# Optimization experiments

Hardware: AMD Instinct MI355X
Metric: run time of the kernel (lower is better)

The kernel has to match this reference:

```python
import jax, jax.numpy as jnp
import numpy as np

K_ORDER = 3
GRID_N = 10
GRID_LO, GRID_HI = -2.0, 2.0
LAYERS = [(49, 256), (256, 256), (256, 10)]
NCOEF = GRID_N + K_ORDER  # 13


def mish(x):
    return x * jnp.tanh(jax.nn.softplus(x))


def bspline_basis(x):
    # x: (B, in) -> basis (B, in, GRID_N + K_ORDER)
    h = (GRID_HI - GRID_LO) / GRID_N
    knots = GRID_LO + h * jnp.arange(-K_ORDER, GRID_N + K_ORDER + 1, dtype=x.dtype)  # (G+2k+1,)
    xx = x[..., None]
    B = ((xx >= knots[:-1]) & (xx < knots[1:])).astype(x.dtype)  # degree-0, (B,in,G+2k)
    for d in range(1, K_ORDER + 1):
        left = (xx - knots[: -(d + 1)]) / (knots[d:-1] - knots[: -(d + 1)]) * B[..., :-1]
        right = (knots[d + 1:] - xx) / (knots[d + 1:] - knots[1:-d]) * B[..., 1:]
        B = left + right
    return B  # (B, in, G+k)


def kan_layer(x, coef, scale_base, scale_sp, bias):
    # x: (B,in); coef: (in,out,G+k); scales: (in,out); bias: (out,)
    basis = bspline_basis(x)                                   # (B,in,G+k)
    spline = jnp.einsum('big,iog->bo', basis, coef * scale_sp[..., None])
    base = jnp.einsum('bi,io->bo', mish(x), scale_base)
    return base + spline + bias


def setup_inputs() -> dict:
    key = jax.random.key(0)
    ks = jax.random.split(key, 1 + 4 * len(LAYERS))
    inp = {'x': jax.random.normal(ks[0], (8192, 1, 28, 28), dtype=jnp.float32)}
    i = 1
    for li, (fin, fout) in enumerate(LAYERS, start=1):
        inp[f'coef{li}'] = 0.1 * jax.random.normal(ks[i], (fin, fout, NCOEF), dtype=jnp.float32); i += 1
        inp[f'sb{li}'] = 1.0 + 0.1 * jax.random.normal(ks[i], (fin, fout), dtype=jnp.float32); i += 1
        inp[f'sp{li}'] = 1.0 + 0.1 * jax.random.normal(ks[i], (fin, fout), dtype=jnp.float32); i += 1
        inp[f'b{li}'] = jnp.zeros((fout,), dtype=jnp.float32); i += 1
    return inp


def reference(x, coef1, sb1, sp1, b1, coef2, sb2, sp2, b2, coef3, sb3, sp3, b3):
    B = x.shape[0]
    # avg_pool2d(x, 4): 28x28 -> 7x7
    h = x.reshape(B, 1, 7, 4, 7, 4).mean(axis=(3, 5))
    h = h.reshape(B, 49)
    h = kan_layer(h, coef1, sb1, sp1, b1)
    h = kan_layer(h, coef2, sb2, sp2, b2)
    h = kan_layer(h, coef3, sb3, sp3, b3)
    return jax.nn.log_softmax(h, axis=1)
```

## Files before the change

kernel.cpp:

```cpp
#include <hip/hip_runtime.h>
#include <hip/hip_bf16.h>

typedef __bf16 bf16x8_t __attribute__((ext_vector_type(8)));
typedef float f32x4_t __attribute__((ext_vector_type(4)));
using bf16 = __hip_bfloat16;

__device__ __forceinline__ unsigned short f2bf_bits(float v) {
  __hip_bfloat16 h = __float2bfloat16(v);
  return *reinterpret_cast<unsigned short*>(&h);
}

__device__ __forceinline__ float mish_f(float x) {
  float z = __expf(x);
  float n = z * (z + 2.0f);
  float m = x * n / (n + 2.0f);
  return (x > 10.0f) ? x : m;
}

__device__ __forceinline__ void kan_feats28(bf16* dst, float x) {
  unsigned int* d32 = (unsigned int*)dst;
#pragma unroll
  for (int d = 0; d < 7; ++d) d32[d] = 0u;
  float t = (x + 3.2f) * 2.5f;
  if (t >= 0.0f && t < 16.0f) {
    float tf = floorf(t);
    int c = (int)tf;
    float u = t - tf;
    float um = 1.0f - u;
    float u2 = u * u, u3 = u2 * u;
    const float s6 = 1.0f / 6.0f;
    float w0 = um * um * um * s6;
    float w1 = (3.0f * u3 - 6.0f * u2 + 4.0f) * s6;
    float w2 = (-3.0f * u3 + 3.0f * u2 + 3.0f * u + 1.0f) * s6;
    float w3 = u3 * s6;
    int j0 = c - 3;
    if (j0 >= 0)               dst[j0]     = __float2bfloat16(w0);
    if (j0 >= -1 && j0 <= 11)  dst[j0 + 1] = __float2bfloat16(w1);
    if (j0 >= -2 && j0 <= 10)  dst[j0 + 2] = __float2bfloat16(w2);
    if (j0 <= 9)               dst[j0 + 3] = __float2bfloat16(w3);
  }
  dst[13] = __float2bfloat16(mish_f(x));
}

__global__ __launch_bounds__(256) void prep_all(
    const float* __restrict__ c1, const float* __restrict__ sb1, const float* __restrict__ sp1,
    const float* __restrict__ c2, const float* __restrict__ sb2, const float* __restrict__ sp2,
    const float* __restrict__ c3, const float* __restrict__ sb3, const float* __restrict__ sp3,
    bf16* __restrict__ W1f, bf16* __restrict__ W2f, bf16* __restrict__ W3f) {
  const int b = blockIdx.x, o = threadIdx.x;
  float vals[14];
  const int ntg = o >> 4, lrr = o & 15;
  if (b < 49) {
    const int i = b;
    const size_t io = (size_t)i * 256 + o;
    const float spv = sp1[io];
#pragma unroll
    for (int r = 0; r < 13; ++r) vals[r] = c1[io * 13 + r] * spv;
    vals[13] = sb1[io];
#pragma unroll
    for (int d = 0; d < 7; ++d) {
      const int k2 = i * 14 + 2 * d;
      const int s = k2 >> 5, r2 = k2 & 31;
      const size_t off = ((size_t)(s * 16 + ntg)) * 512 + lrr * 32 + (r2 >> 3) * 8 + (r2 & 7);
      *(unsigned int*)(W1f + off) = (unsigned int)f2bf_bits(vals[2 * d]) |
                                    ((unsigned int)f2bf_bits(vals[2 * d + 1]) << 16);
    }
  } else if (b == 49) {
#pragma unroll
    for (int d = 0; d < 9; ++d) {
      const int k2 = 686 + 2 * d;
      const int r2 = k2 & 31;
      *(unsigned int*)(W1f + ((size_t)(21 * 16 + ntg)) * 512 + lrr * 32 + (r2 >> 3) * 8 + (r2 & 7)) = 0u;
    }
  } else if (b < 306) {
    const int i = b - 50;
    const size_t io = (size_t)i * 256 + o;
    const float spv = sp2[io];
#pragma unroll
    for (int r = 0; r < 13; ++r) vals[r] = c2[io * 13 + r] * spv;
    vals[13] = sb2[io];
#pragma unroll
    for (int d = 0; d < 7; ++d) {
      const int k2 = i * 14 + 2 * d;
      const int s = k2 >> 5, r2 = k2 & 31;
      const size_t off = ((size_t)(s * 16 + ntg)) * 512 + lrr * 32 + (r2 >> 3) * 8 + (r2 & 7);
      *(unsigned int*)(W2f + off) = (unsigned int)f2bf_bits(vals[2 * d]) |
                                    ((unsigned int)f2bf_bits(vals[2 * d + 1]) << 16);
    }
  } else {
    const int i = b - 306;
    if (o < 10) {
      const size_t io = (size_t)i * 10 + o;
      const float spv = sp3[io];
#pragma unroll
      for (int r = 0; r < 13; ++r) vals[r] = c3[io * 13 + r] * spv;
      vals[13] = sb3[io];
#pragma unroll
      for (int d = 0; d < 7; ++d) {
        const int k2 = i * 14 + 2 * d;
        const int s = k2 >> 5, r2 = k2 & 31;
        const size_t off = (size_t)s * 512 + o * 32 + (r2 >> 3) * 8 + (r2 & 7);
        *(unsigned int*)(W3f + off) = (unsigned int)f2bf_bits(vals[2 * d]) |
                                      ((unsigned int)f2bf_bits(vals[2 * d + 1]) << 16);
      }
    } else if (o < 16) {
#pragma unroll
      for (int d = 0; d < 7; ++d) {
        const int k2 = i * 14 + 2 * d;
        const int s = k2 >> 5, r2 = k2 & 31;
        *(unsigned int*)(W3f + (size_t)s * 512 + o * 32 + (r2 >> 3) * 8 + (r2 & 7)) = 0u;
      }
    }
  }
}

__global__ __launch_bounds__(1024, 4) void meganet(
    const float* __restrict__ x, const bf16* __restrict__ W1f,
    const bf16* __restrict__ W2f, const bf16* __restrict__ W3f,
    const float* __restrict__ b1, const float* __restrict__ b2,
    const float* __restrict__ b3, float* __restrict__ out) {
  __shared__ __align__(16) char lds[126976];
  float* const Hs0 = (float*)lds;
  float* const Hs1 = (float*)(lds + 36864);
  bf16* const Ach0 = (bf16*)(lds + 73728);
  bf16* const Ach1 = (bf16*)(lds + 88576);
  float* const P = (float*)(lds + 103424);
  float* const xs = (float*)lds;
  float* const Red = (float*)(lds + 110592);
  float* const V = (float*)(lds + 124928);

  const int t = threadIdx.x;
  const int w = t >> 6, lane = t & 63, quad = lane >> 4, lr = lane & 15;
  const int tr = (t >> 4) & 31, ej = t & 15;
  const int r0 = blockIdx.x * 32;
  const int foff = lr * 32 + quad * 8;
  const int kg = w >> 3, ng = w & 7;
  const int ntg0 = 2 * ng;
  const int nks = kg ? 3 : 4, ks0 = kg ? 4 : 0;

  for (int h = 0; h < 2; ++h) {
    const float4* src = (const float4*)x + (size_t)(r0 + h * 16) * 196;
    float4* xd = (float4*)xs;
#pragma unroll
    for (int l = 0; l < 4; ++l) {
      const int idx = t + l * 1024;
      if (idx < 3136) xd[idx] = src[idx];
    }
    __syncthreads();
    if (t < 784) {
      const int img = t / 49, p = t - img * 49;
      const int oh = p / 7, ow = p - oh * 7;
      const float* xi = xs + img * 784 + oh * 112 + ow * 4;
      float s = 0.f;
#pragma unroll
      for (int rr = 0; rr < 4; ++rr)
#pragma unroll
        for (int cc = 0; cc < 4; ++cc) s += xi[rr * 28 + cc];
      P[(h * 16 + img) * 56 + p] = s * (1.0f / 16.0f);
    }
    __syncthreads();
  }

  f32x4_t acc[2][2];
#pragma unroll
  for (int m = 0; m < 2; ++m)
#pragma unroll
    for (int n = 0; n < 2; ++n) acc[m][n] = (f32x4_t){0.f, 0.f, 0.f, 0.f};

  bf16x8_t q0[4], q1[4];
  if (kg == 0) {
#pragma unroll
    for (int s = 0; s < 4; ++s) {
      q0[s] = *(const bf16x8_t*)(W1f + (size_t)(s * 16 + ntg0) * 512 + foff);
      q1[s] = *(const bf16x8_t*)(W1f + (size_t)(s * 16 + ntg0 + 1) * 512 + foff);
    }
  }
  if (t >= 512) kan_feats28(Ach0 + tr * 232 + ej * 14, P[tr * 56 + ej]);
  __syncthreads();
#pragma unroll
  for (int c = 0; c < 4; ++c) {
    const bf16* const Ac = (c & 1) ? Ach1 : Ach0;
    bf16* const An = (c & 1) ? Ach0 : Ach1;
    const int nksc = (c < 3) ? 7 : 1;
    if (kg == 0) {
#pragma unroll
      for (int ks = 0; ks < 7; ++ks) {
        if (ks >= nksc) continue;
        const int kk = c * 7 + ks;
        const int sl = kk & 3;
        bf16x8_t bb0 = q0[sl], bb1 = q1[sl];
        if (kk + 4 < 22) {
          q0[sl] = *(const bf16x8_t*)(W1f + (size_t)((kk + 4) * 16 + ntg0) * 512 + foff);
          q1[sl] = *(const bf16x8_t*)(W1f + (size_t)((kk + 4) * 16 + ntg0 + 1) * 512 + foff);
        }
#pragma unroll
        for (int m = 0; m < 2; ++m) {
          bf16x8_t a = *(const bf16x8_t*)(Ac + (m * 16 + lr) * 232 + ks * 32 + quad * 8);
          acc[m][0] = __builtin_amdgcn_mfma_f32_16x16x32_bf16(a, bb0, acc[m][0], 0, 0, 0);
          acc[m][1] = __builtin_amdgcn_mfma_f32_16x16x32_bf16(a, bb1, acc[m][1], 0, 0, 0);
        }
      }
    }
    if (t >= 512) {
      if (c < 2) {
        kan_feats28(An + tr * 232 + ej * 14, P[tr * 56 + (c + 1) * 16 + ej]);
      } else if (c == 2) {
        if (ej == 0) kan_feats28(An + tr * 232, P[tr * 56 + 48]);
        else if (ej == 1) {
          unsigned int* z = (unsigned int*)(An + tr * 232 + 14);
#pragma unroll
          for (int d = 0; d < 9; ++d) z[d] = 0u;
        }
      }
    }
    __syncthreads();
  }
  if (kg == 0) {
#pragma unroll
    for (int m = 0; m < 2; ++m)
#pragma unroll
      for (int n = 0; n < 2; ++n) {
        const int col = ng * 32 + n * 16 + lr;
        const float bn = b1[col];
        f32x4_t v;
#pragma unroll
        for (int r = 0; r < 4; ++r) v[r] = acc[m][n][r] + bn;
        *(f32x4_t*)(Hs0 + col * 36 + m * 16 + quad * 4) = v;
      }
  }
  __syncthreads();

#pragma unroll
  for (int m = 0; m < 2; ++m)
#pragma unroll
    for (int n = 0; n < 2; ++n) acc[m][n] = (f32x4_t){0.f, 0.f, 0.f, 0.f};
  bf16x8_t c0[4], c1[4];
#pragma unroll
  for (int j = 0; j < 4; ++j) {
    if (j < nks) {
      const int kk = ks0 + j;
      c0[j] = *(const bf16x8_t*)(W2f + (size_t)(kk * 16 + ntg0) * 512 + foff);
      c1[j] = *(const bf16x8_t*)(W2f + (size_t)(kk * 16 + ntg0 + 1) * 512 + foff);
    }
  }
  if (t >= 512) kan_feats28(Ach0 + tr * 232 + ej * 14, Hs0[ej * 36 + tr]);
  __syncthreads();
#pragma unroll
  for (int c = 0; c < 16; ++c) {
    const bf16* const Ac = (c & 1) ? Ach1 : Ach0;
    bf16* const An = (c & 1) ? Ach0 : Ach1;
#pragma unroll
    for (int j = 0; j < 4; ++j) {
      if (j >= nks) continue;
      const int kk = c * 7 + ks0 + j;
      bf16x8_t bb0 = c0[j], bb1 = c1[j];
      if (c < 15) {
        c0[j] = *(const bf16x8_t*)(W2f + (size_t)((kk + 7) * 16 + ntg0) * 512 + foff);
        c1[j] = *(const bf16x8_t*)(W2f + (size_t)((kk + 7) * 16 + ntg0 + 1) * 512 + foff);
      }
#pragma unroll
      for (int m = 0; m < 2; ++m) {
        bf16x8_t a = *(const bf16x8_t*)(Ac + (m * 16 + lr) * 232 + (ks0 + j) * 32 + quad * 8);
        acc[m][0] = __builtin_amdgcn_mfma_f32_16x16x32_bf16(a, bb0, acc[m][0], 0, 0, 0);
        acc[m][1] = __builtin_amdgcn_mfma_f32_16x16x32_bf16(a, bb1, acc[m][1], 0, 0, 0);
      }
    }
    if (t >= 512 && c < 15)
      kan_feats28(An + tr * 232 + ej * 14, Hs0[((c + 1) * 16 + ej) * 36 + tr]);
    __syncthreads();
  }
  {
    float* const Hd = kg ? Hs1 : Hs0;
#pragma unroll
    for (int m = 0; m < 2; ++m)
#pragma unroll
      for (int n = 0; n < 2; ++n) {
        const int col = ng * 32 + n * 16 + lr;
        const float bn = kg ? 0.f : b2[col];
        f32x4_t v;
#pragma unroll
        for (int r = 0; r < 4; ++r) v[r] = acc[m][n][r] + bn;
        *(f32x4_t*)(Hd + col * 36 + m * 16 + quad * 4) = v;
      }
  }
  __syncthreads();

  f32x4_t acc3 = {0.f, 0.f, 0.f, 0.f};
  const int mh = w / 7, ks3 = w % 7;
  bf16x8_t q3[2];
  if (w < 14) {
    q3[0] = *(const bf16x8_t*)(W3f + (size_t)ks3 * 512 + foff);
    q3[1] = *(const bf16x8_t*)(W3f + (size_t)(7 + ks3) * 512 + foff);
  }
  if (t < 512) kan_feats28(Ach0 + tr * 232 + ej * 14, Hs0[ej * 36 + tr] + Hs1[ej * 36 + tr]);
  __syncthreads();
#pragma unroll
  for (int c = 0; c < 16; ++c) {
    const bf16* const Ac = (c & 1) ? Ach1 : Ach0;
    bf16* const An = (c & 1) ? Ach0 : Ach1;
    if (w < 14) {
      bf16x8_t bb = q3[c & 1];
      if (c + 2 < 16)
        q3[c & 1] = *(const bf16x8_t*)(W3f + (size_t)((c + 2) * 7 + ks3) * 512 + foff);
      bf16x8_t a = *(const bf16x8_t*)(Ac + (mh * 16 + lr) * 232 + ks3 * 32 + quad * 8);
      acc3 = __builtin_amdgcn_mfma_f32_16x16x32_bf16(a, bb, acc3, 0, 0, 0);
    }
    if (t < 512 && c < 15) {
      const int idx = ((c + 1) * 16 + ej) * 36 + tr;
      kan_feats28(An + tr * 232 + ej * 14, Hs0[idx] + Hs1[idx]);
    }
    __syncthreads();
  }
  if (w < 14) {
#pragma unroll
    for (int r = 0; r < 4; ++r)
      Red[w * 256 + (quad * 4 + r) * 16 + lr] = acc3[r];
  }
  __syncthreads();
  if (t < 512) {
    float s = (ej < 10) ? b3[ej] : 0.f;
    const int mh2 = tr >> 4, lrow = tr & 15;
#pragma unroll
    for (int ks = 0; ks < 7; ++ks) s += Red[(mh2 * 7 + ks) * 256 + lrow * 16 + ej];
    V[tr * 16 + ej] = s;
  }
  __syncthreads();
  if (t < 32) {
    float vv[10];
#pragma unroll
    for (int o = 0; o < 10; ++o) vv[o] = V[t * 16 + o];
    float mx = vv[0];
#pragma unroll
    for (int o = 1; o < 10; ++o) mx = fmaxf(mx, vv[o]);
    float se = 0.f;
#pragma unroll
    for (int o = 0; o < 10; ++o) se += expf(vv[o] - mx);
    const float l = mx + logf(se);
#pragma unroll
    for (int o = 0; o < 10; ++o) out[(size_t)(r0 + t) * 10 + o] = vv[o] - l;
  }
}

extern "C" void kernel_launch(void* const* d_in, const int* in_sizes, int n_in,
                              void* d_out, int out_size, void* d_ws, size_t ws_size,
                              hipStream_t stream) {
  const float* x = (const float*)d_in[0];
  const float* coef1 = (const float*)d_in[1];
  const float* sb1 = (const float*)d_in[2];
  const float* sp1 = (const float*)d_in[3];
  const float* b1 = (const float*)d_in[4];
  const float* coef2 = (const float*)d_in[5];
  const float* sb2 = (const float*)d_in[6];
  const float* sp2 = (const float*)d_in[7];
  const float* b2 = (const float*)d_in[8];
  const float* coef3 = (const float*)d_in[9];
  const float* sb3 = (const float*)d_in[10];
  const float* sp3 = (const float*)d_in[11];
  const float* b3 = (const float*)d_in[12];
  float* out = (float*)d_out;

  char* ws = (char*)d_ws;
  bf16* W1f = (bf16*)ws;
  bf16* W2f = (bf16*)(ws + 360448);
  bf16* W3f = (bf16*)(ws + 2195456);

  prep_all<<<562, 256, 0, stream>>>(coef1, sb1, sp1, coef2, sb2, sp2,
                                    coef3, sb3, sp3, W1f, W2f, W3f);
  meganet<<<256, 1024, 0, stream>>>(x, W1f, W2f, W3f, b1, b2, b3, out);
}
```

Before: 142.4 us.

## Double A-chunk width in layers 2/3 to halve K-chunks and barriers

Widens the LDS feature chunk buffers so each chunk holds 32 input features (476-element row stride) instead of 16 for layers 2 and 3. All 1024 threads now build features, the K-loop runs 8 chunks instead of 16, and each K-group wave does 7 k-steps per chunk with a rotating 4-deep weight prefetch. This halves the number of __syncthreads and feature-build phases. In exchange it raises LDS use, remaps buffers (P/Red/V overlapped), and pools the input in four quarters.

```diff
diff --git a/kernel.cpp b/kernel.cpp
--- a/kernel.cpp
+++ b/kernel.cpp
@@ -119,35 +119,36 @@
     const bf16* __restrict__ W2f, const bf16* __restrict__ W3f,
     const float* __restrict__ b1, const float* __restrict__ b2,
     const float* __restrict__ b3, float* __restrict__ out) {
-  __shared__ __align__(16) char lds[126976];
+  __shared__ __align__(16) char lds[134656];
   float* const Hs0 = (float*)lds;
   float* const Hs1 = (float*)(lds + 36864);
+  float* const P = (float*)(lds + 36864);
+  float* const xs = (float*)lds;
   bf16* const Ach0 = (bf16*)(lds + 73728);
-  bf16* const Ach1 = (bf16*)(lds + 88576);
-  float* const P = (float*)(lds + 103424);
-  float* const xs = (float*)lds;
-  float* const Red = (float*)(lds + 110592);
-  float* const V = (float*)(lds + 124928);
+  bf16* const Ach1 = (bf16*)(lds + 104192);
+  float* const Red = (float*)(lds + 73728);
+  float* const V = (float*)(lds + 104192);
 
   const int t = threadIdx.x;
   const int w = t >> 6, lane = t & 63, quad = lane >> 4, lr = lane & 15;
-  const int tr = (t >> 4) & 31, ej = t & 15;
   const int r0 = blockIdx.x * 32;
   const int foff = lr * 32 + quad * 8;
   const int kg = w >> 3, ng = w & 7;
   const int ntg0 = 2 * ng;
-  const int nks = kg ? 3 : 4, ks0 = kg ? 4 : 0;
-
-  for (int h = 0; h < 2; ++h) {
-    const float4* src = (const float4*)x + (size_t)(r0 + h * 16) * 196;
+  const int ks0 = kg * 7;
+  const int tr16 = (t >> 4) & 31, ej16 = t & 15;
+  const int tr32 = t >> 5, ij = t & 31;
+
+  for (int h = 0; h < 4; ++h) {
+    const float4* src = (const float4*)x + (size_t)(r0 + h * 8) * 196;
     float4* xd = (float4*)xs;
 #pragma unroll
-    for (int l = 0; l < 4; ++l) {
+    for (int l = 0; l < 2; ++l) {
       const int idx = t + l * 1024;
-      if (idx < 3136) xd[idx] = src[idx];
-    }
-    __syncthreads();
-    if (t < 784) {
+      if (idx < 1568) xd[idx] = src[idx];
+    }
+    __syncthreads();
+    if (t < 392) {
       const int img = t / 49, p = t - img * 49;
       const int oh = p / 7, ow = p - oh * 7;
       const float* xi = xs + img * 784 + oh * 112 + ow * 4;
@@ -156,7 +157,7 @@
       for (int rr = 0; rr < 4; ++rr)
 #pragma unroll
         for (int cc = 0; cc < 4; ++cc) s += xi[rr * 28 + cc];
-      P[(h * 16 + img) * 56 + p] = s * (1.0f / 16.0f);
+      P[(h * 8 + img) * 56 + p] = s * (1.0f / 16.0f);
     }
     __syncthreads();
   }
@@ -175,7 +176,7 @@
       q1[s] = *(const bf16x8_t*)(W1f + (size_t)(s * 16 + ntg0 + 1) * 512 + foff);
     }
   }
-  if (t >= 512) kan_feats28(Ach0 + tr * 232 + ej * 14, P[tr * 56 + ej]);
+  if (t >= 512) kan_feats28(Ach0 + tr16 * 476 + ej16 * 14, P[tr16 * 56 + ej16]);
   __syncthreads();
 #pragma unroll
   for (int c = 0; c < 4; ++c) {
@@ -195,7 +196,7 @@
         }
 #pragma unroll
         for (int m = 0; m < 2; ++m) {
-          bf16x8_t a = *(const bf16x8_t*)(Ac + (m * 16 + lr) * 232 + ks * 32 + quad * 8);
+          bf16x8_t a = *(const bf16x8_t*)(Ac + (m * 16 + lr) * 476 + ks * 32 + quad * 8);
           acc[m][0] = __builtin_amdgcn_mfma_f32_16x16x32_bf16(a, bb0, acc[m][0], 0, 0, 0);
           acc[m][1] = __builtin_amdgcn_mfma_f32_16x16x32_bf16(a, bb1, acc[m][1], 0, 0, 0);
         }
@@ -203,11 +204,11 @@
     }
     if (t >= 512) {
       if (c < 2) {
-        kan_feats28(An + tr * 232 + ej * 14, P[tr * 56 + (c + 1) * 16 + ej]);
+        kan_feats28(An + tr16 * 476 + ej16 * 14, P[tr16 * 56 + (c + 1) * 16 + ej16]);
       } else if (c == 2) {
-        if (ej == 0) kan_feats28(An + tr * 232, P[tr * 56 + 48]);
-        else if (ej == 1) {
-          unsigned int* z = (unsigned int*)(An + tr * 232 + 14);
+        if (ej16 == 0) kan_feats28(An + tr16 * 476, P[tr16 * 56 + 48]);
+        else if (ej16 == 1) {
+          unsigned int* z = (unsigned int*)(An + tr16 * 476 + 14);
 #pragma unroll
           for (int d = 0; d < 9; ++d) z[d] = 0u;
         }
@@ -234,39 +235,37 @@
   for (int m = 0; m < 2; ++m)
 #pragma unroll
     for (int n = 0; n < 2; ++n) acc[m][n] = (f32x4_t){0.f, 0.f, 0.f, 0.f};
-  bf16x8_t c0[4], c1[4];
-#pragma unroll
-  for (int j = 0; j < 4; ++j) {
-    if (j < nks) {
-      const int kk = ks0 + j;
-      c0[j] = *(const bf16x8_t*)(W2f + (size_t)(kk * 16 + ntg0) * 512 + foff);
-      c1[j] = *(const bf16x8_t*)(W2f + (size_t)(kk * 16 + ntg0 + 1) * 512 + foff);
-    }
-  }
-  if (t >= 512) kan_feats28(Ach0 + tr * 232 + ej * 14, Hs0[ej * 36 + tr]);
-  __syncthreads();
-#pragma unroll
-  for (int c = 0; c < 16; ++c) {
+#pragma unroll
+  for (int s = 0; s < 4; ++s) {
+    q0[s] = *(const bf16x8_t*)(W2f + (size_t)((ks0 + s) * 16 + ntg0) * 512 + foff);
+    q1[s] = *(const bf16x8_t*)(W2f + (size_t)((ks0 + s) * 16 + ntg0 + 1) * 512 + foff);
+  }
+  kan_feats28(Ach0 + tr32 * 476 + ij * 14, Hs0[ij * 36 + tr32]);
+  __syncthreads();
+#pragma unroll
+  for (int c = 0; c < 8; ++c) {
     const bf16* const Ac = (c & 1) ? Ach1 : Ach0;
     bf16* const An = (c & 1) ? Ach0 : Ach1;
 #pragma unroll
-    for (int j = 0; j < 4; ++j) {
-      if (j >= nks) continue;
-      const int kk = c * 7 + ks0 + j;
-      bf16x8_t bb0 = c0[j], bb1 = c1[j];
-      if (c < 15) {
-        c0[j] = *(const bf16x8_t*)(W2f + (size_t)((kk + 7) * 16 + ntg0) * 512 + foff);
-        c1[j] = *(const bf16x8_t*)(W2f + (size_t)((kk + 7) * 16 + ntg0 + 1) * 512 + foff);
+    for (int j = 0; j < 7; ++j) {
+      const int s = c * 7 + j;
+      const int sl = s & 3;
+      bf16x8_t bb0 = q0[sl], bb1 = q1[sl];
+      if (s + 4 < 56) {
+        const int s2 = s + 4;
+        const int kk2 = (s2 / 7) * 14 + ks0 + (s2 % 7);
+        q0[sl] = *(const bf16x8_t*)(W2f + (size_t)(kk2 * 16 + ntg0) * 512 + foff);
+        q1[sl] = *(const bf16x8_t*)(W2f + (size_t)(kk2 * 16 + ntg0 + 1) * 512 + foff);
       }
 #pragma unroll
       for (int m = 0; m < 2; ++m) {
-        bf16x8_t a = *(const bf16x8_t*)(Ac + (m * 16 + lr) * 232 + (ks0 + j) * 32 + quad * 8);
+        bf16x8_t a = *(const bf16x8_t*)(Ac + (m * 16 + lr) * 476 + (ks0 + j) * 32 + quad * 8);
         acc[m][0] = __builtin_amdgcn_mfma_f32_16x16x32_bf16(a, bb0, acc[m][0], 0, 0, 0);
         acc[m][1] = __builtin_amdgcn_mfma_f32_16x16x32_bf16(a, bb1, acc[m][1], 0, 0, 0);
       }
     }
-    if (t >= 512 && c < 15)
-      kan_feats28(An + tr * 232 + ej * 14, Hs0[((c + 1) * 16 + ej) * 36 + tr]);
+    if (c < 7)
+      kan_feats28(An + tr32 * 476 + ij * 14, Hs0[((c + 1) * 32 + ij) * 36 + tr32]);
     __syncthreads();
   }
   {
@@ -292,22 +291,26 @@
     q3[0] = *(const bf16x8_t*)(W3f + (size_t)ks3 * 512 + foff);
     q3[1] = *(const bf16x8_t*)(W3f + (size_t)(7 + ks3) * 512 + foff);
   }
-  if (t < 512) kan_feats28(Ach0 + tr * 232 + ej * 14, Hs0[ej * 36 + tr] + Hs1[ej * 36 + tr]);
-  __syncthreads();
-#pragma unroll
-  for (int c = 0; c < 16; ++c) {
+  kan_feats28(Ach0 + tr32 * 476 + ij * 14, Hs0[ij * 36 + tr32] + Hs1[ij * 36 + tr32]);
+  __syncthreads();
+#pragma unroll
+  for (int c = 0; c < 8; ++c) {
     const bf16* const Ac = (c & 1) ? Ach1 : Ach0;
     bf16* const An = (c & 1) ? Ach0 : Ach1;
     if (w < 14) {
-      bf16x8_t bb = q3[c & 1];
-      if (c + 2 < 16)
-        q3[c & 1] = *(const bf16x8_t*)(W3f + (size_t)((c + 2) * 7 + ks3) * 512 + foff);
-      bf16x8_t a = *(const bf16x8_t*)(Ac + (mh * 16 + lr) * 232 + ks3 * 32 + quad * 8);
-      acc3 = __builtin_amdgcn_mfma_f32_16x16x32_bf16(a, bb, acc3, 0, 0, 0);
-    }
-    if (t < 512 && c < 15) {
-      const int idx = ((c + 1) * 16 + ej) * 36 + tr;
-      kan_feats28(An + tr * 232 + ej * 14, Hs0[idx] + Hs1[idx]);
+      bf16x8_t bb0 = q3[0], bb1 = q3[1];
+      if (c + 1 < 8) {
+        q3[0] = *(const bf16x8_t*)(W3f + (size_t)((c + 1) * 14 + ks3) * 512 + foff);
+        q3[1] = *(const bf16x8_t*)(W3f + (size_t)((c + 1) * 14 + 7 + ks3) * 512 + foff);
+      }
+      bf16x8_t a0 = *(const bf16x8_t*)(Ac + (mh * 16 + lr) * 476 + ks3 * 32 + quad * 8);
+      bf16x8_t a1 = *(const bf16x8_t*)(Ac + (mh * 16 + lr) * 476 + (7 + ks3) * 32 + quad * 8);
+      acc3 = __builtin_amdgcn_mfma_f32_16x16x32_bf16(a0, bb0, acc3, 0, 0, 0);
+      acc3 = __builtin_amdgcn_mfma_f32_16x16x32_bf16(a1, bb1, acc3, 0, 0, 0);
+    }
+    if (c < 7) {
+      const int idx = ((c + 1) * 32 + ij) * 36 + tr32;
+      kan_feats28(An + tr32 * 476 + ij * 14, Hs0[idx] + Hs1[idx]);
     }
     __syncthreads();
   }
@@ -318,6 +321,7 @@
   }
   __syncthreads();
   if (t < 512) {
+    const int tr = (t >> 4) & 31, ej = t & 15;
     float s = (ej < 10) ? b3[ej] : 0.f;
     const int mh2 = tr >> 4, lrow = tr & 15;
 #pragma unroll
```

Measured after the change: 180.3 us. 1.27x slower.
